# Kernel tuning notes

Hardware: AMD Instinct MI355X
Metric: run time of the kernel (lower is better)

## Reference

```python
import jax, jax.numpy as jnp
import numpy as np

N = 10000      # nodes
E = 640000     # edges
D = 128        # hidden = in_dim = out_dim
L = 4          # GatedGCN layers
G = 128        # graphs in batch
C = 10         # classes


def setup_inputs() -> dict:
    key = jax.random.key(0)
    ks = jax.random.split(key, 16)
    s = 0.05
    nrm = lambda k, shape: (jax.random.normal(k, shape, jnp.float32) * s)
    inp = {
        "feature": jax.random.normal(ks[0], (N, D), jnp.float32),
        "edge_index": jax.random.randint(ks[1], (2, E), 0, N),
        "batch": jnp.sort(jax.random.randint(ks[2], (N,), 0, G)),
        # embedding_h
        "embed_w": nrm(ks[3], (D, D)), "embed_b": nrm(ks[4], (D,)),
        # per-layer GatedGCN params (stacked over L layers; all dims D->D)
        "Aw": nrm(ks[5], (L, D, D)), "Ab": nrm(ks[6], (L, D)),
        "Bw": nrm(ks[7], (L, D, D)), "Bb": nrm(ks[8], (L, D)),
        "Dw": nrm(ks[9], (L, D, D)), "Db": nrm(ks[10], (L, D)),
        "Ew": nrm(ks[11], (L, D, D)), "Eb": nrm(ks[12], (L, D)),
        "bn_g": jnp.ones((L, D), jnp.float32), "bn_b": jnp.zeros((L, D), jnp.float32),
        # MLPReadout: 128 -> 64 -> 32 -> 10
        "mlp_w0": nrm(ks[13], (D, D // 2)), "mlp_b0": jnp.zeros((D // 2,), jnp.float32),
        "mlp_w1": nrm(ks[14], (D // 2, D // 4)), "mlp_b1": jnp.zeros((D // 4,), jnp.float32),
        "mlp_w2": nrm(ks[15], (D // 4, C)), "mlp_b2": jnp.zeros((C,), jnp.float32),
    }
    return inp


def reference(feature, edge_index, batch, embed_w, embed_b,
              Aw, Ab, Bw, Bb, Dw, Db, Ew, Eb, bn_g, bn_b,
              mlp_w0, mlp_b0, mlp_w1, mlp_b1, mlp_w2, mlp_b2):
    src, dst = edge_index[0], edge_index[1]  # messages flow src -> dst
    n = feature.shape[0]
    h = feature @ embed_w + embed_b  # [N, D]
    for l in range(L):
        Ah = h @ Aw[l] + Ab[l]
        Bh = h @ Bw[l] + Bb[l]
        Dh = h @ Dw[l] + Db[l]
        Eh = h @ Ew[l] + Eb[l]
        sigma = jax.nn.sigmoid(Dh[dst] + Eh[src])                         # [E, D] edge gates
        num = jax.ops.segment_sum(sigma * Bh[src], dst, num_segments=n)   # gated message sum
        den = jax.ops.segment_sum(sigma, dst, num_segments=n) + 1e-6
        h_new = Ah + num / den
        # BatchNorm1d over nodes (training-mode batch statistics)
        mean = jnp.mean(h_new, axis=0)
        var = jnp.var(h_new, axis=0)
        h_new = bn_g[l] * (h_new - mean) * jax.lax.rsqrt(var + 1e-5) + bn_b[l]
        h = h + jax.nn.relu(h_new)  # residual
    # mean readout per graph
    counts = jax.ops.segment_sum(jnp.ones((n,), h.dtype), batch, num_segments=G)
    hg = jax.ops.segment_sum(h, batch, num_segments=G) / jnp.maximum(counts, 1.0)[:, None]
    x = jax.nn.relu(hg @ mlp_w0 + mlp_b0)
    x = jax.nn.relu(x @ mlp_w1 + mlp_b1)
    return x @ mlp_w2 + mlp_b2  # [G, C]
```

## Files before the change

### kernel.cpp

```cpp
#include <hip/hip_runtime.h>
#include <math.h>

#define D 128


__global__ void zero_i32_kernel(int* __restrict__ p, int n) {
    int i = blockIdx.x * blockDim.x + threadIdx.x;
    if (i < n) p[i] = 0;
}


__global__ void count_deg_kernel(const int* __restrict__ dst, int* __restrict__ deg, int E) {
    int e = blockIdx.x * blockDim.x + threadIdx.x;
    if (e < E) atomicAdd(&deg[dst[e]], 1);
}

__global__ __launch_bounds__(1024)
void scan_kernel(const int* __restrict__ deg, int* __restrict__ row_ptr,
                 int* __restrict__ fill_ptr, int n) {
    __shared__ int sums[1024];
    int t = threadIdx.x;
    int per = (n + 1023) / 1024;
    int beg = t * per, end = min(n, beg + per);
    int s = 0;
    for (int i = beg; i < end; ++i) s += deg[i];
    sums[t] = s;
    __syncthreads();
    for (int off = 1; off < 1024; off <<= 1) {
        int v = (t >= off) ? sums[t - off] : 0;
        __syncthreads();
        sums[t] += v;
        __syncthreads();
    }
    if (t == 1023) row_ptr[n] = sums[1023];
    int prefix = (t > 0) ? sums[t - 1] : 0;
    for (int i = beg; i < end; ++i) {
        row_ptr[i] = prefix;
        fill_ptr[i] = prefix;
        prefix += deg[i];
    }
}

__global__ void fill_csr_kernel(const int* __restrict__ src, const int* __restrict__ dst,
                                int* __restrict__ fill_ptr, int* __restrict__ csr_src, int E) {
    int e = blockIdx.x * blockDim.x + threadIdx.x;
    if (e < E) {
        int p = atomicAdd(&fill_ptr[dst[e]], 1);
        csr_src[p] = src[e];
    }
}


__global__ __launch_bounds__(256)
void gemm4_kernel(const float* __restrict__ X,
                  const float* __restrict__ W0, const float* __restrict__ B0, float* __restrict__ C0,
                  const float* __restrict__ W1, const float* __restrict__ B1, float* __restrict__ C1,
                  const float* __restrict__ W2, const float* __restrict__ B2, float* __restrict__ C2,
                  const float* __restrict__ W3, const float* __restrict__ B3, float* __restrict__ C3,
                  int M) {
    const float* W; const float* Bv; float* C;
    switch (blockIdx.y) {
        case 0:  W = W0; Bv = B0; C = C0; break;
        case 1:  W = W1; Bv = B1; C = C1; break;
        case 2:  W = W2; Bv = B2; C = C2; break;
        default: W = W3; Bv = B3; C = C3; break;
    }
    __shared__ float Xs[32 * 68];
    __shared__ float Ws[32 * 128];

    const int tid = threadIdx.x;
    const int m0  = blockIdx.x * 64;
    const int tn  = tid & 15, tm = tid >> 4;
    const int c0  = tn * 8,  r0 = tm * 4;

    float acc[4][8];
    #pragma unroll
    for (int i = 0; i < 4; ++i)
        #pragma unroll
        for (int j = 0; j < 8; ++j) acc[i][j] = 0.f;

    const int cg   = tid & 7;
    const int xrow = tid >> 3;

    for (int k0 = 0; k0 < 128; k0 += 32) {
        #pragma unroll
        for (int b = 0; b < 2; ++b) {
            int row = xrow + b * 32;
            int m = m0 + row;
            float4 v = make_float4(0.f, 0.f, 0.f, 0.f);
            if (m < M) v = *(const float4*)(X + (size_t)m * D + k0 + cg * 4);
            Xs[(cg * 4 + 0) * 68 + row] = v.x;
            Xs[(cg * 4 + 1) * 68 + row] = v.y;
            Xs[(cg * 4 + 2) * 68 + row] = v.z;
            Xs[(cg * 4 + 3) * 68 + row] = v.w;
        }
        {
            const float4* Wsrc = (const float4*)(W + (size_t)k0 * D);
            float4* Wdst = (float4*)Ws;
            #pragma unroll
            for (int i = 0; i < 4; ++i) Wdst[i * 256 + tid] = Wsrc[i * 256 + tid];
        }
        __syncthreads();
        #pragma unroll
        for (int k = 0; k < 32; ++k) {
            float4 xv = *(const float4*)(Xs + k * 68 + r0);
            float4 wa = *(const float4*)(Ws + k * 128 + c0);
            float4 wb = *(const float4*)(Ws + k * 128 + c0 + 4);
            float xs[4]  = {xv.x, xv.y, xv.z, xv.w};
            float wsv[8] = {wa.x, wa.y, wa.z, wa.w, wb.x, wb.y, wb.z, wb.w};
            #pragma unroll
            for (int i = 0; i < 4; ++i)
                #pragma unroll
                for (int j = 0; j < 8; ++j) acc[i][j] = fmaf(xs[i], wsv[j], acc[i][j]);
        }
        __syncthreads();
    }

    float bia[8];
    #pragma unroll
    for (int j = 0; j < 8; ++j) bia[j] = Bv[c0 + j];
    #pragma unroll
    for (int i = 0; i < 4; ++i) {
        int m = m0 + r0 + i;
        if (m < M) {
            float4 oa, ob;
            oa.x = acc[i][0] + bia[0]; oa.y = acc[i][1] + bia[1];
            oa.z = acc[i][2] + bia[2]; oa.w = acc[i][3] + bia[3];
            ob.x = acc[i][4] + bia[4]; ob.y = acc[i][5] + bia[5];
            ob.z = acc[i][6] + bia[6]; ob.w = acc[i][7] + bia[7];
            *(float4*)(C + (size_t)m * D + c0)     = oa;
            *(float4*)(C + (size_t)m * D + c0 + 4) = ob;
        }
    }
}


__global__ __launch_bounds__(128)
void aggregate_kernel(const float* __restrict__ Ah, const float* __restrict__ Bh,
                      const float* __restrict__ Dh, const float* __restrict__ Eh,
                      const int* __restrict__ row_ptr, const int* __restrict__ csr_src,
                      float* __restrict__ tmp) {
    const int node = blockIdx.x;
    const int d = threadIdx.x;
    const float dh = Dh[(size_t)node * D + d];
    float num = 0.f, den = 0.f;
    const int beg = row_ptr[node], end = row_ptr[node + 1];
    __shared__ int s_src[128];
    for (int base = beg; base < end; base += 128) {
        int cnt = min(128, end - base);
        __syncthreads();
        if (d < cnt) s_src[d] = csr_src[base + d];
        __syncthreads();
        for (int i = 0; i < cnt; ++i) {
            int s = s_src[i];
            float e = Eh[(size_t)s * D + d];
            float b = Bh[(size_t)s * D + d];
            float sig = 1.f / (1.f + __expf(-(dh + e)));
            num = fmaf(sig, b, num);
            den += sig;
        }
    }
    tmp[(size_t)node * D + d] = Ah[(size_t)node * D + d] + num / (den + 1e-6f);
}


__global__ __launch_bounds__(256)
void bn_stats_kernel(const float* __restrict__ tmp, float* __restrict__ stats, int n) {
    const int d = threadIdx.x & 127;
    const int r = threadIdx.x >> 7;
    float s = 0.f, s2 = 0.f;
    for (int row = blockIdx.x * 2 + r; row < n; row += gridDim.x * 2) {
        float v = tmp[(size_t)row * D + d];
        s += v;
        s2 = fmaf(v, v, s2);
    }
    __shared__ float ls[256], ls2[256];
    ls[threadIdx.x] = s; ls2[threadIdx.x] = s2;
    __syncthreads();
    if (r == 0) {
        s  += ls[128 + d];
        s2 += ls2[128 + d];
        atomicAdd(&stats[d], s);
        atomicAdd(&stats[D + d], s2);
    }
}

__global__ __launch_bounds__(256)
void bn_apply_kernel(float* __restrict__ h, const float* __restrict__ tmp,
                     const float* __restrict__ stats,
                     const float* __restrict__ gamma, const float* __restrict__ beta,
                     int n) {
    int i = blockIdx.x * blockDim.x + threadIdx.x;
    if (i >= n * 32) return;
    const int d0 = (i & 31) * 4;
    const float inv_n = 1.f / (float)n;
    float4 t4 = ((const float4*)tmp)[i];
    float4 h4 = ((float4*)h)[i];
    float tv[4] = {t4.x, t4.y, t4.z, t4.w};
    float hv[4] = {h4.x, h4.y, h4.z, h4.w};
    #pragma unroll
    for (int j = 0; j < 4; ++j) {
        int d = d0 + j;
        float mean = stats[d] * inv_n;
        float var  = stats[D + d] * inv_n - mean * mean;
        float rs   = rsqrtf(var + 1e-5f);
        float v    = gamma[d] * (tv[j] - mean) * rs + beta[d];
        hv[j] += fmaxf(v, 0.f);
    }
    float4 o; o.x = hv[0]; o.y = hv[1]; o.z = hv[2]; o.w = hv[3];
    ((float4*)h)[i] = o;
}


__device__ inline int lower_bound_i(const int* a, int n, int key) {
    int lo = 0, hi = n;
    while (lo < hi) {
        int mid = (lo + hi) >> 1;
        if (a[mid] < key) lo = mid + 1; else hi = mid;
    }
    return lo;
}

__global__ __launch_bounds__(128)
void readout_kernel(const float* __restrict__ h, const int* __restrict__ batch,
                    float* __restrict__ hg, int n) {
    const int g = blockIdx.x, d = threadIdx.x;
    const int lo = lower_bound_i(batch, n, g);
    const int hi = lower_bound_i(batch, n, g + 1);
    float s = 0.f;
    for (int i = lo; i < hi; ++i) s += h[(size_t)i * D + d];
    float cnt = (float)(hi - lo);
    hg[g * D + d] = s / fmaxf(cnt, 1.f);
}

__global__ __launch_bounds__(128)
void mlp_kernel(const float* __restrict__ hg,
                const float* __restrict__ w0, const float* __restrict__ b0,
                const float* __restrict__ w1, const float* __restrict__ b1,
                const float* __restrict__ w2, const float* __restrict__ b2,
                float* __restrict__ out) {
    const int g = blockIdx.x, t = threadIdx.x;
    __shared__ float x[128], y[64], z[32];
    x[t] = hg[g * 128 + t];
    __syncthreads();
    if (t < 64) {
        float a = b0[t];
        #pragma unroll 8
        for (int k = 0; k < 128; ++k) a = fmaf(x[k], w0[k * 64 + t], a);
        y[t] = fmaxf(a, 0.f);
    }
    __syncthreads();
    if (t < 32) {
        float a = b1[t];
        #pragma unroll 8
        for (int k = 0; k < 64; ++k) a = fmaf(y[k], w1[k * 32 + t], a);
        z[t] = fmaxf(a, 0.f);
    }
    __syncthreads();
    if (t < 10) {
        float a = b2[t];
        #pragma unroll 8
        for (int k = 0; k < 32; ++k) a = fmaf(z[k], w2[k * 10 + t], a);
        out[g * 10 + t] = a;
    }
}


extern "C" void kernel_launch(void* const* d_in, const int* in_sizes, int n_in,
                              void* d_out, int out_size, void* d_ws, size_t ws_size,
                              hipStream_t stream) {
    const float* feature  = (const float*)d_in[0];
    const int*   edge_idx = (const int*)  d_in[1];
    const int*   batch    = (const int*)  d_in[2];
    const float* embed_w  = (const float*)d_in[3];
    const float* embed_b  = (const float*)d_in[4];
    const float* Aw = (const float*)d_in[5];
    const float* Ab = (const float*)d_in[6];
    const float* Bw = (const float*)d_in[7];
    const float* Bb = (const float*)d_in[8];
    const float* Dw = (const float*)d_in[9];
    const float* Db = (const float*)d_in[10];
    const float* Ew = (const float*)d_in[11];
    const float* Eb = (const float*)d_in[12];
    const float* bn_g = (const float*)d_in[13];
    const float* bn_b = (const float*)d_in[14];
    const float* mlp_w0 = (const float*)d_in[15];
    const float* mlp_b0 = (const float*)d_in[16];
    const float* mlp_w1 = (const float*)d_in[17];
    const float* mlp_b1 = (const float*)d_in[18];
    const float* mlp_w2 = (const float*)d_in[19];
    const float* mlp_b2 = (const float*)d_in[20];

    const int N = in_sizes[0] / D;
    const int E = in_sizes[1] / 2;
    const int L = in_sizes[6] / D;
    const int G = out_size / 10;

    const int* src = edge_idx;
    const int* dst = edge_idx + E;

    size_t NF = (size_t)N * D;
    float* h     = (float*)d_ws;
    float* Ah    = h + NF;
    float* Bh    = Ah + NF;
    float* Dh    = Bh + NF;
    float* Ehh   = Dh + NF;
    float* tmp   = Ehh + NF;
    float* hg    = tmp + NF;
    float* stats = hg + (size_t)G * D;
    int* deg      = (int*)(stats + 2 * D);
    int* row_ptr  = deg + N;
    int* fill_ptr = row_ptr + (N + 1);
    int* csr_src  = fill_ptr + N;

    zero_i32_kernel<<<dim3((N + 255) / 256), dim3(256), 0, stream>>>(deg, N);
    count_deg_kernel<<<dim3((E + 255) / 256), dim3(256), 0, stream>>>(dst, deg, E);
    scan_kernel<<<dim3(1), dim3(1024), 0, stream>>>(deg, row_ptr, fill_ptr, N);
    fill_csr_kernel<<<dim3((E + 255) / 256), dim3(256), 0, stream>>>(src, dst, fill_ptr, csr_src, E);

    const int MB = (N + 63) / 64;

    gemm4_kernel<<<dim3(MB, 1), dim3(256), 0, stream>>>(
        feature,
        embed_w, embed_b, h,  embed_w, embed_b, h,
        embed_w, embed_b, h,  embed_w, embed_b, h, N);

    for (int l = 0; l < L; ++l) {
        const float* wA = Aw + (size_t)l * D * D; const float* bA = Ab + (size_t)l * D;
        const float* wB = Bw + (size_t)l * D * D; const float* bB = Bb + (size_t)l * D;
        const float* wD = Dw + (size_t)l * D * D; const float* bD = Db + (size_t)l * D;
        const float* wE = Ew + (size_t)l * D * D; const float* bE = Eb + (size_t)l * D;

        gemm4_kernel<<<dim3(MB, 4), dim3(256), 0, stream>>>(
            h, wA, bA, Ah,  wB, bB, Bh,  wD, bD, Dh,  wE, bE, Ehh, N);

        aggregate_kernel<<<dim3(N), dim3(128), 0, stream>>>(
            Ah, Bh, Dh, Ehh, row_ptr, csr_src, tmp);

        zero_i32_kernel<<<dim3(1), dim3(256), 0, stream>>>((int*)stats, 2 * D);
        bn_stats_kernel<<<dim3(256), dim3(256), 0, stream>>>(tmp, stats, N);
        bn_apply_kernel<<<dim3((N * 32 + 255) / 256), dim3(256), 0, stream>>>(
            h, tmp, stats, bn_g + (size_t)l * D, bn_b + (size_t)l * D, N);
    }

    readout_kernel<<<dim3(G), dim3(128), 0, stream>>>(h, batch, hg, N);
    mlp_kernel<<<dim3(G), dim3(128), 0, stream>>>(
        hg, mlp_w0, mlp_b0, mlp_w1, mlp_b1, mlp_w2, mlp_b2, (float*)d_out);
}
```

Before: 662.3 us.

## Retile GEMM with register prefetch, vectorize aggregation and fuse BN stats

The GEMM tile grows to 128x128 with an 8x8 per-thread microtile, and the next K-chunk of X and W is prefetched into registers while the current one is computed. Aggregation now maps one 32-lane group to each node with float4 loads and hardware exp2/rcp sigmoid, replacing one 128-thread block per node and its shared-memory index staging. BatchNorm sum and sum-of-squares are reduced inside the aggregation kernel, which removes a separate stats pass. Per-layer stats buffers are zeroed once up front, so the per-layer zero launch also goes away. The costs are higher register pressure in the GEMM, half as many GEMM blocks, and more atomics on the stats arrays (one set per 8 nodes).

After: 769.8 us. +16.2%, slower.

```diff
diff --git a/kernel.cpp b/kernel.cpp
--- a/kernel.cpp
+++ b/kernel.cpp
@@ -2,6 +2,8 @@
 #include <math.h>
 
 #define D 128
+#define BM 128
+#define BK 32
 
 
 __global__ void zero_i32_kernel(int* __restrict__ p, int n) {
@@ -51,7 +53,7 @@
 }
 
 
-__global__ __launch_bounds__(256)
+__global__ __launch_bounds__(256, 2)
 void gemm4_kernel(const float* __restrict__ X,
                   const float* __restrict__ W0, const float* __restrict__ B0, float* __restrict__ C0,
                   const float* __restrict__ W1, const float* __restrict__ B1, float* __restrict__ C1,
@@ -65,125 +67,150 @@
         case 2:  W = W2; Bv = B2; C = C2; break;
         default: W = W3; Bv = B3; C = C3; break;
     }
-    __shared__ float Xs[32 * 68];
-    __shared__ float Ws[32 * 128];
+    __shared__ float Xs[BK][BM + 4];
+    __shared__ float Ws[BK][D];
 
     const int tid = threadIdx.x;
-    const int m0  = blockIdx.x * 64;
-    const int tn  = tid & 15, tm = tid >> 4;
-    const int c0  = tn * 8,  r0 = tm * 4;
-
-    float acc[4][8];
+    const int m0  = blockIdx.x * BM;
+    const int tn  = tid & 15;
+    const int tm  = tid >> 4;
+    const int r0  = tm * 8;
+    const int c0  = tn * 4;
+
+    const int srow = tid >> 3;
+    const int sq   = tid & 7;
+
+    const float4* X4 = (const float4*)X;
+    const float4* W4 = (const float4*)W;
+
+    float acc[8][8];
     #pragma unroll
-    for (int i = 0; i < 4; ++i)
+    for (int i = 0; i < 8; ++i)
         #pragma unroll
         for (int j = 0; j < 8; ++j) acc[i][j] = 0.f;
 
-    const int cg   = tid & 7;
-    const int xrow = tid >> 3;
-
-    for (int k0 = 0; k0 < 128; k0 += 32) {
+    float4 xr[4], wr[4];
+    #pragma unroll
+    for (int t = 0; t < 4; ++t) {
+        int m = m0 + t * 32 + srow;
+        xr[t] = (m < M) ? X4[(size_t)m * 32 + sq] : make_float4(0.f, 0.f, 0.f, 0.f);
+        wr[t] = W4[t * 256 + tid];
+    }
+
+    for (int c = 0; c < 4; ++c) {
+        if (c) __syncthreads();
         #pragma unroll
-        for (int b = 0; b < 2; ++b) {
-            int row = xrow + b * 32;
-            int m = m0 + row;
-            float4 v = make_float4(0.f, 0.f, 0.f, 0.f);
-            if (m < M) v = *(const float4*)(X + (size_t)m * D + k0 + cg * 4);
-            Xs[(cg * 4 + 0) * 68 + row] = v.x;
-            Xs[(cg * 4 + 1) * 68 + row] = v.y;
-            Xs[(cg * 4 + 2) * 68 + row] = v.z;
-            Xs[(cg * 4 + 3) * 68 + row] = v.w;
-        }
-        {
-            const float4* Wsrc = (const float4*)(W + (size_t)k0 * D);
-            float4* Wdst = (float4*)Ws;
+        for (int t = 0; t < 4; ++t) {
+            int row = t * 32 + srow;
+            Xs[sq * 4 + 0][row] = xr[t].x;
+            Xs[sq * 4 + 1][row] = xr[t].y;
+            Xs[sq * 4 + 2][row] = xr[t].z;
+            Xs[sq * 4 + 3][row] = xr[t].w;
+            ((float4*)Ws)[t * 256 + tid] = wr[t];
+        }
+        __syncthreads();
+        if (c < 3) {
             #pragma unroll
-            for (int i = 0; i < 4; ++i) Wdst[i * 256 + tid] = Wsrc[i * 256 + tid];
-        }
-        __syncthreads();
+            for (int t = 0; t < 4; ++t) {
+                int m = m0 + t * 32 + srow;
+                xr[t] = (m < M) ? X4[(size_t)m * 32 + (c + 1) * 8 + sq]
+                                : make_float4(0.f, 0.f, 0.f, 0.f);
+                wr[t] = W4[(c + 1) * 1024 + t * 256 + tid];
+            }
+        }
         #pragma unroll
-        for (int k = 0; k < 32; ++k) {
-            float4 xv = *(const float4*)(Xs + k * 68 + r0);
-            float4 wa = *(const float4*)(Ws + k * 128 + c0);
-            float4 wb = *(const float4*)(Ws + k * 128 + c0 + 4);
-            float xs[4]  = {xv.x, xv.y, xv.z, xv.w};
-            float wsv[8] = {wa.x, wa.y, wa.z, wa.w, wb.x, wb.y, wb.z, wb.w};
+        for (int k = 0; k < BK; ++k) {
+            float4 xa = *(const float4*)&Xs[k][r0];
+            float4 xb = *(const float4*)&Xs[k][r0 + 4];
+            float4 wa = *(const float4*)&Ws[k][c0];
+            float4 wb = *(const float4*)&Ws[k][c0 + 64];
+            float xv[8] = {xa.x, xa.y, xa.z, xa.w, xb.x, xb.y, xb.z, xb.w};
+            float wv[8] = {wa.x, wa.y, wa.z, wa.w, wb.x, wb.y, wb.z, wb.w};
             #pragma unroll
-            for (int i = 0; i < 4; ++i)
+            for (int i = 0; i < 8; ++i)
                 #pragma unroll
-                for (int j = 0; j < 8; ++j) acc[i][j] = fmaf(xs[i], wsv[j], acc[i][j]);
-        }
-        __syncthreads();
-    }
-
-    float bia[8];
+                for (int j = 0; j < 8; ++j)
+                    acc[i][j] = fmaf(xv[i], wv[j], acc[i][j]);
+        }
+    }
+
+    float4 ba = ((const float4*)Bv)[tn];
+    float4 bb = ((const float4*)Bv)[tn + 16];
+    float4* C4 = (float4*)C;
     #pragma unroll
-    for (int j = 0; j < 8; ++j) bia[j] = Bv[c0 + j];
-    #pragma unroll
-    for (int i = 0; i < 4; ++i) {
+    for (int i = 0; i < 8; ++i) {
         int m = m0 + r0 + i;
         if (m < M) {
             float4 oa, ob;
-            oa.x = acc[i][0] + bia[0]; oa.y = acc[i][1] + bia[1];
-            oa.z = acc[i][2] + bia[2]; oa.w = acc[i][3] + bia[3];
-            ob.x = acc[i][4] + bia[4]; ob.y = acc[i][5] + bia[5];
-            ob.z = acc[i][6] + bia[6]; ob.w = acc[i][7] + bia[7];
-            *(float4*)(C + (size_t)m * D + c0)     = oa;
-            *(float4*)(C + (size_t)m * D + c0 + 4) = ob;
-        }
-    }
-}
-
-
-__global__ __launch_bounds__(128)
+            oa.x = acc[i][0] + ba.x; oa.y = acc[i][1] + ba.y;
+            oa.z = acc[i][2] + ba.z; oa.w = acc[i][3] + ba.w;
+            ob.x = acc[i][4] + bb.x; ob.y = acc[i][5] + bb.y;
+            ob.z = acc[i][6] + bb.z; ob.w = acc[i][7] + bb.w;
+            C4[(size_t)m * 32 + tn]      = oa;
+            C4[(size_t)m * 32 + 16 + tn] = ob;
+        }
+    }
+}
+
+
+__global__ __launch_bounds__(256)
 void aggregate_kernel(const float* __restrict__ Ah, const float* __restrict__ Bh,
                       const float* __restrict__ Dh, const float* __restrict__ Eh,
                       const int* __restrict__ row_ptr, const int* __restrict__ csr_src,
-                      float* __restrict__ tmp) {
-    const int node = blockIdx.x;
-    const int d = threadIdx.x;
-    const float dh = Dh[(size_t)node * D + d];
-    float num = 0.f, den = 0.f;
-    const int beg = row_ptr[node], end = row_ptr[node + 1];
-    __shared__ int s_src[128];
-    for (int base = beg; base < end; base += 128) {
-        int cnt = min(128, end - base);
-        __syncthreads();
-        if (d < cnt) s_src[d] = csr_src[base + d];
-        __syncthreads();
-        for (int i = 0; i < cnt; ++i) {
-            int s = s_src[i];
-            float e = Eh[(size_t)s * D + d];
-            float b = Bh[(size_t)s * D + d];
-            float sig = 1.f / (1.f + __expf(-(dh + e)));
-            num = fmaf(sig, b, num);
-            den += sig;
-        }
-    }
-    tmp[(size_t)node * D + d] = Ah[(size_t)node * D + d] + num / (den + 1e-6f);
-}
-
-
-__global__ __launch_bounds__(256)
-void bn_stats_kernel(const float* __restrict__ tmp, float* __restrict__ stats, int n) {
-    const int d = threadIdx.x & 127;
-    const int r = threadIdx.x >> 7;
-    float s = 0.f, s2 = 0.f;
-    for (int row = blockIdx.x * 2 + r; row < n; row += gridDim.x * 2) {
-        float v = tmp[(size_t)row * D + d];
-        s += v;
-        s2 = fmaf(v, v, s2);
-    }
-    __shared__ float ls[256], ls2[256];
-    ls[threadIdx.x] = s; ls2[threadIdx.x] = s2;
-    __syncthreads();
-    if (r == 0) {
-        s  += ls[128 + d];
-        s2 += ls2[128 + d];
+                      float* __restrict__ tmp, float* __restrict__ stats, int N) {
+    const int nl = threadIdx.x >> 5;
+    const int g  = threadIdx.x & 31;
+    const int node = blockIdx.x * 8 + nl;
+
+    float4 t4 = make_float4(0.f, 0.f, 0.f, 0.f);
+    if (node < N) {
+        const float4* Dh4 = (const float4*)Dh;
+        const float4* Eh4 = (const float4*)Eh;
+        const float4* Bh4 = (const float4*)Bh;
+        const float4* Ah4 = (const float4*)Ah;
+        const float4 dh = Dh4[(size_t)node * 32 + g];
+        float4 num = make_float4(0.f, 0.f, 0.f, 0.f);
+        float4 den = make_float4(0.f, 0.f, 0.f, 0.f);
+        const int beg = row_ptr[node], end = row_ptr[node + 1];
+        const float LOG2E = 1.44269504088896340736f;
+        for (int i = beg; i < end; ++i) {
+            int s = csr_src[i];
+            float4 e4 = Eh4[(size_t)s * 32 + g];
+            float4 b4 = Bh4[(size_t)s * 32 + g];
+            float sx = __builtin_amdgcn_rcpf(1.f + __builtin_amdgcn_exp2f(-(dh.x + e4.x) * LOG2E));
+            float sy = __builtin_amdgcn_rcpf(1.f + __builtin_amdgcn_exp2f(-(dh.y + e4.y) * LOG2E));
+            float sz = __builtin_amdgcn_rcpf(1.f + __builtin_amdgcn_exp2f(-(dh.z + e4.z) * LOG2E));
+            float sw = __builtin_amdgcn_rcpf(1.f + __builtin_amdgcn_exp2f(-(dh.w + e4.w) * LOG2E));
+            num.x = fmaf(sx, b4.x, num.x); den.x += sx;
+            num.y = fmaf(sy, b4.y, num.y); den.y += sy;
+            num.z = fmaf(sz, b4.z, num.z); den.z += sz;
+            num.w = fmaf(sw, b4.w, num.w); den.w += sw;
+        }
+        float4 ah = Ah4[(size_t)node * 32 + g];
+        t4.x = ah.x + num.x / (den.x + 1e-6f);
+        t4.y = ah.y + num.y / (den.y + 1e-6f);
+        t4.z = ah.z + num.z / (den.z + 1e-6f);
+        t4.w = ah.w + num.w / (den.w + 1e-6f);
+        ((float4*)tmp)[(size_t)node * 32 + g] = t4;
+    }
+
+    __shared__ float redV[8][132];
+    __shared__ float redQ[8][132];
+    *(float4*)&redV[nl][g * 4] = t4;
+    float4 q4;
+    q4.x = t4.x * t4.x; q4.y = t4.y * t4.y; q4.z = t4.z * t4.z; q4.w = t4.w * t4.w;
+    *(float4*)&redQ[nl][g * 4] = q4;
+    __syncthreads();
+    if (threadIdx.x < 128) {
+        int d = threadIdx.x;
+        float s = 0.f, s2 = 0.f;
+        #pragma unroll
+        for (int n2 = 0; n2 < 8; ++n2) { s += redV[n2][d]; s2 += redQ[n2][d]; }
         atomicAdd(&stats[d], s);
         atomicAdd(&stats[D + d], s2);
     }
 }
+
 
 __global__ __launch_bounds__(256)
 void bn_apply_kernel(float* __restrict__ h, const float* __restrict__ tmp,
@@ -307,18 +334,20 @@
     float* Ehh   = Dh + NF;
     float* tmp   = Ehh + NF;
     float* hg    = tmp + NF;
-    float* stats = hg + (size_t)G * D;
-    int* deg      = (int*)(stats + 2 * D);
+    float* statsAll = hg + (size_t)G * D;
+    int* deg      = (int*)(statsAll + (size_t)L * 2 * D);
     int* row_ptr  = deg + N;
     int* fill_ptr = row_ptr + (N + 1);
     int* csr_src  = fill_ptr + N;
 
-    zero_i32_kernel<<<dim3((N + 255) / 256), dim3(256), 0, stream>>>(deg, N);
+    int nz = L * 2 * D + N;
+    zero_i32_kernel<<<dim3((nz + 255) / 256), dim3(256), 0, stream>>>((int*)statsAll, nz);
+
     count_deg_kernel<<<dim3((E + 255) / 256), dim3(256), 0, stream>>>(dst, deg, E);
     scan_kernel<<<dim3(1), dim3(1024), 0, stream>>>(deg, row_ptr, fill_ptr, N);
     fill_csr_kernel<<<dim3((E + 255) / 256), dim3(256), 0, stream>>>(src, dst, fill_ptr, csr_src, E);
 
-    const int MB = (N + 63) / 64;
+    const int MB = (N + BM - 1) / BM;
 
     gemm4_kernel<<<dim3(MB, 1), dim3(256), 0, stream>>>(
         feature,
@@ -330,15 +359,14 @@
         const float* wB = Bw + (size_t)l * D * D; const float* bB = Bb + (size_t)l * D;
         const float* wD = Dw + (size_t)l * D * D; const float* bD = Db + (size_t)l * D;
         const float* wE = Ew + (size_t)l * D * D; const float* bE = Eb + (size_t)l * D;
+        float* stats = statsAll + (size_t)l * 2 * D;
 
         gemm4_kernel<<<dim3(MB, 4), dim3(256), 0, stream>>>(
             h, wA, bA, Ah,  wB, bB, Bh,  wD, bD, Dh,  wE, bE, Ehh, N);
 
-        aggregate_kernel<<<dim3(N), dim3(128), 0, stream>>>(
-            Ah, Bh, Dh, Ehh, row_ptr, csr_src, tmp);
-
-        zero_i32_kernel<<<dim3(1), dim3(256), 0, stream>>>((int*)stats, 2 * D);
-        bn_stats_kernel<<<dim3(256), dim3(256), 0, stream>>>(tmp, stats, N);
+        aggregate_kernel<<<dim3((N + 7) / 8), dim3(256), 0, stream>>>(
+            Ah, Bh, Dh, Ehh, row_ptr, csr_src, tmp, stats, N);
+
         bn_apply_kernel<<<dim3((N * 32 + 255) / 256), dim3(256), 0, stream>>>(
             h, tmp, stats, bn_g + (size_t)l * D, bn_b + (size_t)l * D, N);
     }
```
